# Kernel optimization log

Hardware: AMD Instinct MI355X
Metric: run time of the kernel (lower is better)

Reference implementation:

```python
import jax, jax.numpy as jnp
import numpy as np

BN_EPS = 1e-5
B, L, D = 16, 2048, 1024
OS = 64          # attnList[0]
NC = 256         # candidates per sample
CLASS_NUM = 8921
LAB = 1024


def setup_inputs() -> dict:
    key = jax.random.key(0)
    ks = jax.random.split(key, 8)
    scale_a = 1.0 / np.sqrt(D)
    return {
        "X": jax.random.normal(ks[0], (B, L, D), jnp.float32),
        "candidate": jax.random.randint(ks[1], (B, NC), 0, CLASS_NUM, jnp.int64),
        "a_w": jax.random.normal(ks[2], (D, OS), jnp.float32) * scale_a,
        "a_b": jnp.zeros((OS,), jnp.float32),
        "h_w": jax.random.normal(ks[3], (D, LAB), jnp.float32) * scale_a,
        "h_b": jnp.zeros((LAB,), jnp.float32),
        "bn_gamma": jax.random.uniform(ks[4], (LAB,), jnp.float32, 0.5, 1.5),
        "bn_beta": jax.random.normal(ks[5], (LAB,), jnp.float32) * 0.1,
        "bn_mean": jnp.zeros((LAB,), jnp.float32),
        "bn_var": jnp.ones((LAB,), jnp.float32),
        "labDescVec": jax.random.normal(ks[6], (CLASS_NUM, LAB), jnp.float32),
    }


def reference(X, candidate, a_w, a_b, h_w, h_b, bn_gamma, bn_beta, bn_mean, bn_var, labDescVec):
    # --- attention-pooling layer (attnList has one entry) ---
    # alpha: softmax over the sequence dim (dim=1 in torch)
    alpha = jax.nn.softmax(jnp.einsum('bld,do->blo', X, a_w) + a_b, axis=1)  # [B,L,OS]
    Xp = jnp.einsum('blo,bld->bod', alpha, X)                                # [B,OS,D]
    Xp = jnp.einsum('bod,dh->boh', Xp, h_w) + h_b                            # [B,OS,LAB]
    # BatchNorm1d over feature dim (eval mode: running stats)
    Xp = (Xp - bn_mean) * (bn_gamma / jnp.sqrt(bn_var + BN_EPS)) + bn_beta
    Xp = jax.nn.relu(Xp)  # dropout is identity at inference
    # --- candidate attention ---
    batchLabelVec = labDescVec[candidate]                                    # [B,NC,LAB]
    scores = jnp.einsum('boh,bch->boc', Xp, batchLabelVec)                   # [B,OS,NC]
    alpha2 = jax.nn.softmax(scores, axis=1)                                  # softmax over OS (dim=1)
    out = jnp.einsum('boc,boh->bch', alpha2, Xp)                             # [B,NC,LAB]
    return out
```

## Files before the change

kernel.cpp:

```cpp
#include <hip/hip_runtime.h>
#include <hip/hip_bf16.h>
#include <math.h>

#define Bb   16
#define Ll   2048
#define Dd   1024
#define OSo  64
#define NCc  256
#define LABh 1024
#define BN_EPS 1e-5f

typedef short s8v  __attribute__((ext_vector_type(8)));
typedef short s4v  __attribute__((ext_vector_type(4)));
typedef float f32x4 __attribute__((ext_vector_type(4)));

__device__ __forceinline__ short f2b(float f) {
    __hip_bfloat16 h = __float2bfloat16(f);
    short s;
    __builtin_memcpy(&s, &h, 2);
    return s;
}
__device__ __forceinline__ float b2f(short s) {
    union { unsigned u; float f; } v; v.u = ((unsigned)(unsigned short)s) << 16;
    return v.f;
}
__device__ __forceinline__ void fastbar() {
    asm volatile("s_waitcnt lgkmcnt(0)\n\ts_barrier" ::: "memory");
}
__device__ __forceinline__ int swi(int row, int kElem) {
    return (row * 128 + ((kElem * 2) ^ ((row & 7) << 4))) >> 1;
}
__device__ __forceinline__ f32x4 MF(s8v a, s8v b, f32x4 c) {
    return __builtin_amdgcn_mfma_f32_16x16x32_bf16(a, b, c, 0, 0, 0);
}

__global__ __launch_bounds__(256) void k0(const float* __restrict__ h_w,
                                          const float* __restrict__ a_w,
                                          short* __restrict__ h_wT,
                                          short* __restrict__ a_wT) {
    __shared__ float t[64][68];
    const int tid = threadIdx.x, id = blockIdx.x;
    const float* src; short* dst; int srw, d0, y0;
    if (id < 256) { src = h_w; dst = h_wT; srw = LABh; d0 = (id & 15) * 64; y0 = (id >> 4) * 64; }
    else          { src = a_w; dst = a_wT; srw = OSo;  d0 = (id - 256) * 64; y0 = 0; }
    const int r = tid >> 2, cofs = (tid & 3) * 16;
    #pragma unroll
    for (int w = 0; w < 4; ++w) {
        float4 v = *(const float4*)&src[(size_t)(d0 + r) * srw + y0 + cofs + w * 4];
        t[r][cofs + w * 4 + 0] = v.x;
        t[r][cofs + w * 4 + 1] = v.y;
        t[r][cofs + w * 4 + 2] = v.z;
        t[r][cofs + w * 4 + 3] = v.w;
    }
    __syncthreads();
    s8v o0, o1;
    #pragma unroll
    for (int e = 0; e < 8; ++e) { o0[e] = f2b(t[cofs + e][r]); o1[e] = f2b(t[cofs + 8 + e][r]); }
    *(s8v*)&dst[(size_t)(y0 + r) * Dd + d0 + cofs]     = o0;
    *(s8v*)&dst[(size_t)(y0 + r) * Dd + d0 + cofs + 8] = o1;
}

struct R1 { float4 x[4]; s8v w[2]; };

__global__ __launch_bounds__(256) void k1(const float* __restrict__ X,
                                          const short* __restrict__ a_wT,
                                          float* __restrict__ StP) {
    __shared__ __align__(16) char smem[32768];
    float (*ts)[65] = (float(*)[65])smem;
    const int tid = threadIdx.x;
    const int lane = tid & 63, wave = tid >> 6;
    const int wm = wave >> 1, wn = wave & 1;
    const int b = blockIdx.y, l0 = blockIdx.x * 64;
    const int z = blockIdx.z, kbase = z * 512;
    const float* Xb = X + ((size_t)b * Ll + l0) * Dd;
    const int r = tid >> 2, kofs = (tid & 3) * 16;
    f32x4 acc[2][2] = {};
    R1 cur, nxt;
    #pragma unroll
    for (int w = 0; w < 2; ++w) {
        cur.x[2*w]   = *(const float4*)&Xb[(size_t)r * Dd + kbase + kofs + w * 8];
        cur.x[2*w+1] = *(const float4*)&Xb[(size_t)r * Dd + kbase + kofs + w * 8 + 4];
        cur.w[w]     = *(const s8v*)&a_wT[(size_t)r * Dd + kbase + kofs + w * 8];
    }
    #pragma unroll
    for (int t = 0; t < 8; ++t) {
        short* As = (short*)(smem + (t & 1) * 8192);
        short* Bs = (short*)(smem + 16384 + (t & 1) * 8192);
        #pragma unroll
        for (int w = 0; w < 2; ++w) {
            const float* f0 = (const float*)&cur.x[2*w];
            s8v s;
            s[0]=f2b(f0[0]); s[1]=f2b(f0[1]); s[2]=f2b(f0[2]); s[3]=f2b(f0[3]);
            s[4]=f2b(f0[4]); s[5]=f2b(f0[5]); s[6]=f2b(f0[6]); s[7]=f2b(f0[7]);
            *(s8v*)&As[swi(r, kofs + w * 8)] = s;
            *(s8v*)&Bs[swi(r, kofs + w * 8)] = cur.w[w];
        }
        fastbar();
        if (t < 7) {
            const int k0 = kbase + (t + 1) * 64;
            #pragma unroll
            for (int w = 0; w < 2; ++w) {
                nxt.x[2*w]   = *(const float4*)&Xb[(size_t)r * Dd + k0 + kofs + w * 8];
                nxt.x[2*w+1] = *(const float4*)&Xb[(size_t)r * Dd + k0 + kofs + w * 8 + 4];
                nxt.w[w]     = *(const s8v*)&a_wT[(size_t)r * Dd + k0 + kofs + w * 8];
            }
        }
        #pragma unroll
        for (int kk = 0; kk < 2; ++kk) {
            const int kb = kk * 32 + (lane >> 4) * 8;
            s8v a[2], bb[2];
            #pragma unroll
            for (int i = 0; i < 2; ++i)
                a[i] = *(const s8v*)&As[swi(wm * 32 + i * 16 + (lane & 15), kb)];
            #pragma unroll
            for (int j = 0; j < 2; ++j)
                bb[j] = *(const s8v*)&Bs[swi(wn * 32 + j * 16 + (lane & 15), kb)];
            #pragma unroll
            for (int i = 0; i < 2; ++i)
                #pragma unroll
                for (int j = 0; j < 2; ++j)
                    acc[i][j] = MF(a[i], bb[j], acc[i][j]);
        }
        if (t < 7) cur = nxt;
    }
    __syncthreads();
    #pragma unroll
    for (int i = 0; i < 2; ++i)
        #pragma unroll
        for (int j = 0; j < 2; ++j)
            #pragma unroll
            for (int rr = 0; rr < 4; ++rr)
                ts[wm * 32 + i * 16 + (lane >> 4) * 4 + rr][wn * 32 + j * 16 + (lane & 15)] = acc[i][j][rr];
    __syncthreads();
    const int o = tid >> 2, lofs = (tid & 3) * 16;
    float* Sp = StP + (size_t)z * ((size_t)Bb * OSo * Ll)
                    + ((size_t)b * OSo + o) * Ll + l0 + lofs;
    #pragma unroll
    for (int w = 0; w < 4; ++w) {
        float4 v;
        v.x = ts[lofs + w * 4 + 0][o];
        v.y = ts[lofs + w * 4 + 1][o];
        v.z = ts[lofs + w * 4 + 2][o];
        v.w = ts[lofs + w * 4 + 3][o];
        *(float4*)&Sp[w * 4] = v;
    }
}

__global__ __launch_bounds__(256) void k2(const float* __restrict__ StP,
                                          const float* __restrict__ a_b,
                                          short* __restrict__ aBf) {
    __shared__ float row[Ll];
    __shared__ float red[8];
    const size_t ZS = (size_t)Bb * OSo * Ll;
    const float* p0 = StP + (size_t)blockIdx.x * Ll;
    const float* p1 = p0 + ZS;
    short* ab = aBf + (size_t)blockIdx.x * Ll;
    const int tid = threadIdx.x;
    const int wave = tid >> 6, lane = tid & 63;
    const float bias = a_b[blockIdx.x & (OSo - 1)];
    float m = -1e30f;
    for (int i = tid; i < Ll; i += 256) {
        float v = p0[i] + p1[i] + bias;
        row[i] = v; m = fmaxf(m, v);
    }
    #pragma unroll
    for (int off = 32; off; off >>= 1) m = fmaxf(m, __shfl_down(m, off));
    if (lane == 0) red[wave] = m;
    __syncthreads();
    if (tid == 0) red[4] = fmaxf(fmaxf(red[0], red[1]), fmaxf(red[2], red[3]));
    __syncthreads();
    const float M = red[4];
    float s = 0.f;
    for (int i = tid; i < Ll; i += 256) { float e = __expf(row[i] - M); row[i] = e; s += e; }
    __syncthreads();
    #pragma unroll
    for (int off = 32; off; off >>= 1) s += __shfl_down(s, off);
    if (lane == 0) red[wave] = s;
    __syncthreads();
    if (tid == 0) red[4] = 1.f / (red[0] + red[1] + red[2] + red[3]);
    __syncthreads();
    const float inv = red[4];
    for (int i = tid; i < Ll; i += 256) ab[i] = f2b(row[i] * inv);
}

struct R3 { s8v al[2]; float4 xv[4]; };

__global__ __launch_bounds__(256) void k3(const float* __restrict__ X,
                                          const short* __restrict__ aBf,
                                          float* __restrict__ XpP) {
    __shared__ __align__(16) char smem[32768];
    float (*ts)[68] = (float(*)[68])smem;
    const int tid = threadIdx.x;
    const int lane = tid & 63, wave = tid >> 6;
    const int wm = wave >> 1, wn = wave & 1;
    const int id = blockIdx.x;
    const int slot = id >> 3;
    const int b = (id & 7) * 2 + (slot >> 5);
    const int inner = slot & 31;
    const int dt = inner & 15, z = inner >> 4;
    const int d0 = dt * 64;
    const float* Xb = X + (size_t)b * Ll * Dd;
    const short* ab = aBf + (size_t)b * OSo * Ll;
    float* outP = XpP + (size_t)z * ((size_t)Bb * OSo * Dd);
    f32x4 acc[2][2] = {};
    const int arow = tid >> 2, akofs = (tid & 3) * 16;
    const int lq = tid & 15, dq = tid >> 4;
    const int lbase = z * 1024;
    R3 cur, nxt;
    #pragma unroll
    for (int w = 0; w < 2; ++w)
        cur.al[w] = *(const s8v*)&ab[(size_t)arow * Ll + lbase + akofs + w * 8];
    #pragma unroll
    for (int i = 0; i < 4; ++i)
        cur.xv[i] = *(const float4*)&Xb[(size_t)(lbase + lq * 4 + i) * Dd + d0 + dq * 4];
    #pragma unroll
    for (int t = 0; t < 16; ++t) {
        short* Aal = (short*)(smem + (t & 1) * 8192);
        short* Xs  = (short*)(smem + 16384 + (t & 1) * 8192);
        #pragma unroll
        for (int w = 0; w < 2; ++w)
            *(s8v*)&Aal[swi(arow, akofs + w * 8)] = cur.al[w];
        {
            const float* f = (const float*)cur.xv;
            #pragma unroll
            for (int j = 0; j < 4; ++j) {
                const int rowd = dq * 4 + j;
                s4v sj;
                sj[0] = f2b(f[0 * 4 + j]);
                sj[1] = f2b(f[1 * 4 + j]);
                sj[2] = f2b(f[2 * 4 + j]);
                sj[3] = f2b(f[3 * 4 + j]);
                *(s4v*)&Xs[swi(rowd, lq * 4)] = sj;
            }
        }
        fastbar();
        if (t < 15) {
            const int l0 = lbase + (t + 1) * 64;
            #pragma unroll
            for (int w = 0; w < 2; ++w)
                nxt.al[w] = *(const s8v*)&ab[(size_t)arow * Ll + l0 + akofs + w * 8];
            #pragma unroll
            for (int i = 0; i < 4; ++i)
                nxt.xv[i] = *(const float4*)&Xb[(size_t)(l0 + lq * 4 + i) * Dd + d0 + dq * 4];
        }
        #pragma unroll
        for (int kk = 0; kk < 2; ++kk) {
            const int kb = kk * 32 + (lane >> 4) * 8;
            s8v a[2], bb[2];
            #pragma unroll
            for (int i = 0; i < 2; ++i)
                a[i] = *(const s8v*)&Aal[swi(wm * 32 + i * 16 + (lane & 15), kb)];
            #pragma unroll
            for (int j = 0; j < 2; ++j)
                bb[j] = *(const s8v*)&Xs[swi(wn * 32 + j * 16 + (lane & 15), kb)];
            #pragma unroll
            for (int i = 0; i < 2; ++i)
                #pragma unroll
                for (int j = 0; j < 2; ++j)
                    acc[i][j] = MF(a[i], bb[j], acc[i][j]);
        }
        if (t < 15) cur = nxt;
    }
    __syncthreads();
    #pragma unroll
    for (int i = 0; i < 2; ++i)
        #pragma unroll
        for (int j = 0; j < 2; ++j)
            #pragma unroll
            for (int rr = 0; rr < 4; ++rr)
                ts[wm * 32 + i * 16 + (lane >> 4) * 4 + rr][wn * 32 + j * 16 + (lane & 15)] = acc[i][j][rr];
    __syncthreads();
    const int o = tid >> 2, dofs = (tid & 3) * 16;
    float* op = outP + ((size_t)b * OSo + o) * Dd + d0 + dofs;
    #pragma unroll
    for (int w = 0; w < 4; ++w)
        *(float4*)&op[w * 4] = *(float4*)&ts[o][dofs + w * 4];
}

struct R4 { float4 p[8]; s8v w[2]; };

__global__ __launch_bounds__(256) void k4(const float* __restrict__ XpP,
                                          const short* __restrict__ h_wT,
                                          const float* __restrict__ h_b,
                                          const float* __restrict__ gamma,
                                          const float* __restrict__ beta,
                                          const float* __restrict__ mean,
                                          const float* __restrict__ var,
                                          short* __restrict__ Xh) {
    __shared__ __align__(16) char smem[32768];
    short* tsb = (short*)smem;
    const int tid = threadIdx.x, lane = tid & 63, wave = tid >> 6;
    const int wm = wave >> 1, wn = wave & 1;
    const int h0 = blockIdx.x * 64, m0 = blockIdx.y * 64;
    const int r = tid >> 2, kofs = (tid & 3) * 16;
    const size_t ZS = (size_t)Bb * OSo * Dd;
    f32x4 acc[2][2] = {};
    R4 cur, nxt;
    #pragma unroll
    for (int w = 0; w < 2; ++w) {
        const float* p0 = XpP + (size_t)(m0 + r) * Dd + kofs + w * 8;
        cur.p[w*4+0] = *(const float4*)&p0[0];
        cur.p[w*4+1] = *(const float4*)&p0[4];
        cur.p[w*4+2] = *(const float4*)&p0[ZS];
        cur.p[w*4+3] = *(const float4*)&p0[ZS + 4];
        cur.w[w]     = *(const s8v*)&h_wT[(size_t)(h0 + r) * Dd + kofs + w * 8];
    }
    #pragma unroll
    for (int t = 0; t < 16; ++t) {
        short* As = (short*)(smem + (t & 1) * 8192);
        short* Bs = (short*)(smem + 16384 + (t & 1) * 8192);
        #pragma unroll
        for (int w = 0; w < 2; ++w) {
            const float* f0 = (const float*)&cur.p[w*4];
            const float* f1 = (const float*)&cur.p[w*4+2];
            s8v s;
            #pragma unroll
            for (int e = 0; e < 8; ++e) s[e] = f2b(f0[e] + f1[e]);
            *(s8v*)&As[swi(r, kofs + w * 8)] = s;
            *(s8v*)&Bs[swi(r, kofs + w * 8)] = cur.w[w];
        }
        fastbar();
        if (t < 15) {
            const int k0 = (t + 1) * 64;
            #pragma unroll
            for (int w = 0; w < 2; ++w) {
                const float* p0 = XpP + (size_t)(m0 + r) * Dd + k0 + kofs + w * 8;
                nxt.p[w*4+0] = *(const float4*)&p0[0];
                nxt.p[w*4+1] = *(const float4*)&p0[4];
                nxt.p[w*4+2] = *(const float4*)&p0[ZS];
                nxt.p[w*4+3] = *(const float4*)&p0[ZS + 4];
                nxt.w[w]     = *(const s8v*)&h_wT[(size_t)(h0 + r) * Dd + k0 + kofs + w * 8];
            }
        }
        #pragma unroll
        for (int kk = 0; kk < 2; ++kk) {
            const int kb = kk * 32 + (lane >> 4) * 8;
            s8v a[2], bb[2];
            #pragma unroll
            for (int i = 0; i < 2; ++i)
                a[i] = *(const s8v*)&As[swi(wm * 32 + i * 16 + (lane & 15), kb)];
            #pragma unroll
            for (int j = 0; j < 2; ++j)
                bb[j] = *(const s8v*)&Bs[swi(wn * 32 + j * 16 + (lane & 15), kb)];
            #pragma unroll
            for (int i = 0; i < 2; ++i)
                #pragma unroll
                for (int j = 0; j < 2; ++j)
                    acc[i][j] = MF(a[i], bb[j], acc[i][j]);
        }
        if (t < 15) cur = nxt;
    }
    __syncthreads();
    #pragma unroll
    for (int j = 0; j < 2; ++j) {
        const int h = h0 + wn * 32 + j * 16 + (lane & 15);
        const float sc = gamma[h] * rsqrtf(var[h] + BN_EPS);
        const float of = (h_b[h] - mean[h]) * sc + beta[h];
        #pragma unroll
        for (int i = 0; i < 2; ++i)
            #pragma unroll
            for (int rr = 0; rr < 4; ++rr) {
                const int ml = wm * 32 + i * 16 + (lane >> 4) * 4 + rr;
                tsb[ml * 64 + wn * 32 + j * 16 + (lane & 15)] = f2b(fmaxf(0.f, acc[i][j][rr] * sc + of));
            }
    }
    __syncthreads();
    #pragma unroll
    for (int w = 0; w < 2; ++w)
        *(s8v*)&Xh[(size_t)(m0 + r) * LABh + h0 + kofs + w * 8] = *(const s8v*)&tsb[r * 64 + kofs + w * 8];
}

struct R5 { float4 ld[4]; s8v xh[2]; };

__global__ __launch_bounds__(256) void k5(const int* __restrict__ cand,
                                          const float* __restrict__ labD,
                                          const short* __restrict__ Xh,
                                          float* __restrict__ scP) {
    __shared__ __align__(16) char smem[33024];
    float (*ts)[68] = (float(*)[68])smem;
    int* cidx = (int*)(smem + 32768);
    const int tid = threadIdx.x, lane = tid & 63, wave = tid >> 6;
    const int wm = wave >> 1, wn = wave & 1;
    const int b = blockIdx.y;
    const int ct = blockIdx.x & 3, z = blockIdx.x >> 2;
    const int c0 = ct * 64;
    const int kbase = z * 256;
    if (tid < 64) cidx[tid] = cand[b * NCc + c0 + tid];
    __syncthreads();
    const int r = tid >> 2, kofs = (tid & 3) * 16;
    const int ci = cidx[r];
    const float* lrow = labD + (size_t)ci * LABh + kbase;
    const short* xrow = Xh + (size_t)(b * OSo + r) * LABh + kbase;
    f32x4 acc[2][2] = {};
    R5 cur, nxt;
    #pragma unroll
    for (int w = 0; w < 2; ++w) {
        cur.ld[2*w]   = *(const float4*)&lrow[kofs + w * 8];
        cur.ld[2*w+1] = *(const float4*)&lrow[kofs + w * 8 + 4];
        cur.xh[w]     = *(const s8v*)&xrow[kofs + w * 8];
    }
    #pragma unroll
    for (int t = 0; t < 4; ++t) {
        short* As = (short*)(smem + (t & 1) * 8192);
        short* Bs = (short*)(smem + 16384 + (t & 1) * 8192);
        #pragma unroll
        for (int w = 0; w < 2; ++w) {
            const float* f0 = (const float*)&cur.ld[2*w];
            s8v s;
            #pragma unroll
            for (int e = 0; e < 8; ++e) s[e] = f2b(f0[e]);
            *(s8v*)&As[swi(r, kofs + w * 8)] = s;
            *(s8v*)&Bs[swi(r, kofs + w * 8)] = cur.xh[w];
        }
        fastbar();
        if (t < 3) {
            const int k0 = (t + 1) * 64;
            #pragma unroll
            for (int w = 0; w < 2; ++w) {
                nxt.ld[2*w]   = *(const float4*)&lrow[k0 + kofs + w * 8];
                nxt.ld[2*w+1] = *(const float4*)&lrow[k0 + kofs + w * 8 + 4];
                nxt.xh[w]     = *(const s8v*)&xrow[k0 + kofs + w * 8];
            }
        }
        #pragma unroll
        for (int kk = 0; kk < 2; ++kk) {
            const int kb = kk * 32 + (lane >> 4) * 8;
            s8v a[2], bb[2];
            #pragma unroll
            for (int i = 0; i < 2; ++i)
                a[i] = *(const s8v*)&As[swi(wm * 32 + i * 16 + (lane & 15), kb)];
            #pragma unroll
            for (int j = 0; j < 2; ++j)
                bb[j] = *(const s8v*)&Bs[swi(wn * 32 + j * 16 + (lane & 15), kb)];
            #pragma unroll
            for (int i = 0; i < 2; ++i)
                #pragma unroll
                for (int j = 0; j < 2; ++j)
                    acc[i][j] = MF(a[i], bb[j], acc[i][j]);
        }
        if (t < 3) cur = nxt;
    }
    __syncthreads();
    #pragma unroll
    for (int i = 0; i < 2; ++i)
        #pragma unroll
        for (int j = 0; j < 2; ++j)
            #pragma unroll
            for (int rr = 0; rr < 4; ++rr)
                ts[wm * 32 + i * 16 + (lane >> 4) * 4 + rr][wn * 32 + j * 16 + (lane & 15)] = acc[i][j][rr];
    __syncthreads();
    const int oofs = (tid & 3) * 16;
    float* sp = scP + (size_t)z * ((size_t)Bb * NCc * OSo)
                    + ((size_t)b * NCc + c0 + r) * OSo + oofs;
    #pragma unroll
    for (int w = 0; w < 4; ++w)
        *(float4*)&sp[w * 4] = *(float4*)&ts[r][oofs + w * 4];
}

__global__ __launch_bounds__(256) void k6(const float* __restrict__ scP,
                                          const short* __restrict__ Xh,
                                          float* __restrict__ out) {
    __shared__ float al[8][64];
    const int tid = threadIdx.x;
    const int id = blockIdx.x;
    const int slot = id >> 3;
    const int b = (id & 7) * 2 + (slot >> 5);
    const int c0 = (slot & 31) * 8;
    const size_t ZS = (size_t)Bb * NCc * OSo;
    {
        const int cl = tid >> 5, t32 = tid & 31;
        const float* srow = scP + ((size_t)b * NCc + c0 + cl) * OSo;
        float v[2];
        float m = -1e30f;
        #pragma unroll
        for (int j = 0; j < 2; ++j) {
            const int o = t32 + j * 32;
            v[j] = srow[o] + srow[ZS + o] + srow[2 * ZS + o] + srow[3 * ZS + o];
            m = fmaxf(m, v[j]);
        }
        #pragma unroll
        for (int off = 16; off; off >>= 1) m = fmaxf(m, __shfl_xor(m, off, 32));
        float s = 0.f;
        #pragma unroll
        for (int j = 0; j < 2; ++j) { v[j] = __expf(v[j] - m); s += v[j]; }
        #pragma unroll
        for (int off = 16; off; off >>= 1) s += __shfl_xor(s, off, 32);
        float inv = 1.f / s;
        #pragma unroll
        for (int j = 0; j < 2; ++j) al[cl][t32 + j * 32] = v[j] * inv;
    }
    __syncthreads();
    const short* xb = Xh + (size_t)b * OSo * LABh;
    float acc[8][4] = {};
    for (int o = 0; o < OSo; ++o) {
        s4v xv = *(const s4v*)&xb[(size_t)o * LABh + tid * 4];
        const float x0 = b2f(xv[0]), x1 = b2f(xv[1]), x2 = b2f(xv[2]), x3 = b2f(xv[3]);
        #pragma unroll
        for (int c = 0; c < 8; ++c) {
            const float w = al[c][o];
            acc[c][0] += w * x0; acc[c][1] += w * x1; acc[c][2] += w * x2; acc[c][3] += w * x3;
        }
    }
    #pragma unroll
    for (int c = 0; c < 8; ++c) {
        float4 v; v.x = acc[c][0]; v.y = acc[c][1]; v.z = acc[c][2]; v.w = acc[c][3];
        *(float4*)&out[((size_t)b * NCc + c0 + c) * LABh + tid * 4] = v;
    }
}

extern "C" void kernel_launch(void* const* d_in, const int* in_sizes, int n_in,
                              void* d_out, int out_size, void* d_ws, size_t ws_size,
                              hipStream_t stream) {
    (void)in_sizes; (void)n_in; (void)out_size; (void)ws_size;
    const float* X      = (const float*)d_in[0];
    const int*   cand   = (const int*)  d_in[1];
    const float* a_w    = (const float*)d_in[2];
    const float* a_b    = (const float*)d_in[3];
    const float* h_w    = (const float*)d_in[4];
    const float* h_b    = (const float*)d_in[5];
    const float* gamma  = (const float*)d_in[6];
    const float* beta   = (const float*)d_in[7];
    const float* mean   = (const float*)d_in[8];
    const float* var    = (const float*)d_in[9];
    const float* labDesc= (const float*)d_in[10];
    float* outp = (float*)d_out;

    char* ws = (char*)d_ws;
    float* StP  = (float*)ws;
    float* XpP  = (float*)ws;
    short* aBf  = (short*)(ws + ((size_t)16 << 20));
    short* Xh   = (short*)(ws + ((size_t)20 << 20));
    float* scP  = (float*)(ws + ((size_t)22 << 20));
    short* a_wT = (short*)(ws + ((size_t)26 << 20));
    short* h_wT = (short*)(ws + ((size_t)27 << 20));

    k0 <<<272,              256, 0, stream>>>(h_w, a_w, h_wT, a_wT);
    k1 <<<dim3(32, 16, 2),  256, 0, stream>>>(X, a_wT, StP);
    k2 <<<Bb * OSo,         256, 0, stream>>>(StP, a_b, aBf);
    k3 <<<512,              256, 0, stream>>>(X, aBf, XpP);
    k4 <<<dim3(16, 16),     256, 0, stream>>>(XpP, h_wT, h_b, gamma, beta, mean, var, Xh);
    k5 <<<dim3(16, 16),     256, 0, stream>>>(cand, labDesc, Xh, scP);
    k6 <<<512,              256, 0, stream>>>(scP, Xh, outp);
}
```

Baseline: 110.5 us.

## Fuse candidate score GEMM with softmax and weighted sum; vectorize alpha softmax

Merges the candidate-score kernel (k5) and the softmax/weighted-sum kernel (k6) into one kernel, k56. Each block computes scores for 16 candidates over the full LAB dimension, applies softmax over OS in shared memory, and then accumulates the output. This removes the split-K partial score buffer, its global round trip and one launch, at the cost of a small-tile GEMM with only one MFMA per wave per k-step and 256 blocks. The sequence softmax kernel k2 also switches to float4 loads and stores.

Result: faster. 106.2 us (-3.9%).

```diff
diff --git a/kernel.cpp b/kernel.cpp
--- a/kernel.cpp
+++ b/kernel.cpp
@@ -158,10 +158,17 @@
     const int tid = threadIdx.x;
     const int wave = tid >> 6, lane = tid & 63;
     const float bias = a_b[blockIdx.x & (OSo - 1)];
+    const int base = tid * 4;
     float m = -1e30f;
-    for (int i = tid; i < Ll; i += 256) {
-        float v = p0[i] + p1[i] + bias;
-        row[i] = v; m = fmaxf(m, v);
+    #pragma unroll
+    for (int i = base; i < Ll; i += 1024) {
+        float4 a = *(const float4*)&p0[i];
+        float4 c = *(const float4*)&p1[i];
+        float4 v;
+        v.x = a.x + c.x + bias; v.y = a.y + c.y + bias;
+        v.z = a.z + c.z + bias; v.w = a.w + c.w + bias;
+        *(float4*)&row[i] = v;
+        m = fmaxf(m, fmaxf(fmaxf(v.x, v.y), fmaxf(v.z, v.w)));
     }
     #pragma unroll
     for (int off = 32; off; off >>= 1) m = fmaxf(m, __shfl_down(m, off));
@@ -171,7 +178,14 @@
     __syncthreads();
     const float M = red[4];
     float s = 0.f;
-    for (int i = tid; i < Ll; i += 256) { float e = __expf(row[i] - M); row[i] = e; s += e; }
+    #pragma unroll
+    for (int i = base; i < Ll; i += 1024) {
+        float4 v = *(const float4*)&row[i];
+        v.x = __expf(v.x - M); v.y = __expf(v.y - M);
+        v.z = __expf(v.z - M); v.w = __expf(v.w - M);
+        *(float4*)&row[i] = v;
+        s += (v.x + v.y) + (v.z + v.w);
+    }
     __syncthreads();
     #pragma unroll
     for (int off = 32; off; off >>= 1) s += __shfl_down(s, off);
@@ -180,7 +194,14 @@
     if (tid == 0) red[4] = 1.f / (red[0] + red[1] + red[2] + red[3]);
     __syncthreads();
     const float inv = red[4];
-    for (int i = tid; i < Ll; i += 256) ab[i] = f2b(row[i] * inv);
+    #pragma unroll
+    for (int i = base; i < Ll; i += 1024) {
+        float4 v = *(const float4*)&row[i];
+        s4v o;
+        o[0] = f2b(v.x * inv); o[1] = f2b(v.y * inv);
+        o[2] = f2b(v.z * inv); o[3] = f2b(v.w * inv);
+        *(s4v*)&ab[i] = o;
+    }
 }
 
 struct R3 { s8v al[2]; float4 xv[4]; };
@@ -370,141 +391,99 @@
         *(s8v*)&Xh[(size_t)(m0 + r) * LABh + h0 + kofs + w * 8] = *(const s8v*)&tsb[r * 64 + kofs + w * 8];
 }
 
-struct R5 { float4 ld[4]; s8v xh[2]; };
-
-__global__ __launch_bounds__(256) void k5(const int* __restrict__ cand,
-                                          const float* __restrict__ labD,
-                                          const short* __restrict__ Xh,
-                                          float* __restrict__ scP) {
-    __shared__ __align__(16) char smem[33024];
+struct R56 { float4 ld; s8v xh[2]; };
+
+__global__ __launch_bounds__(256) void k56(const int* __restrict__ cand,
+                                           const float* __restrict__ labD,
+                                           const short* __restrict__ Xh,
+                                           float* __restrict__ out) {
+    __shared__ __align__(16) char smem[20608];
     float (*ts)[68] = (float(*)[68])smem;
-    int* cidx = (int*)(smem + 32768);
+    float (*al)[64] = (float(*)[64])(smem + 4608);
+    int* cidx = (int*)(smem + 20480);
     const int tid = threadIdx.x, lane = tid & 63, wave = tid >> 6;
-    const int wm = wave >> 1, wn = wave & 1;
-    const int b = blockIdx.y;
-    const int ct = blockIdx.x & 3, z = blockIdx.x >> 2;
-    const int c0 = ct * 64;
-    const int kbase = z * 256;
-    if (tid < 64) cidx[tid] = cand[b * NCc + c0 + tid];
-    __syncthreads();
-    const int r = tid >> 2, kofs = (tid & 3) * 16;
-    const int ci = cidx[r];
-    const float* lrow = labD + (size_t)ci * LABh + kbase;
-    const short* xrow = Xh + (size_t)(b * OSo + r) * LABh + kbase;
-    f32x4 acc[2][2] = {};
-    R5 cur, nxt;
-    #pragma unroll
-    for (int w = 0; w < 2; ++w) {
-        cur.ld[2*w]   = *(const float4*)&lrow[kofs + w * 8];
-        cur.ld[2*w+1] = *(const float4*)&lrow[kofs + w * 8 + 4];
-        cur.xh[w]     = *(const s8v*)&xrow[kofs + w * 8];
-    }
-    #pragma unroll
-    for (int t = 0; t < 4; ++t) {
-        short* As = (short*)(smem + (t & 1) * 8192);
-        short* Bs = (short*)(smem + 16384 + (t & 1) * 8192);
-        #pragma unroll
-        for (int w = 0; w < 2; ++w) {
-            const float* f0 = (const float*)&cur.ld[2*w];
-            s8v s;
-            #pragma unroll
-            for (int e = 0; e < 8; ++e) s[e] = f2b(f0[e]);
-            *(s8v*)&As[swi(r, kofs + w * 8)] = s;
-            *(s8v*)&Bs[swi(r, kofs + w * 8)] = cur.xh[w];
+    const int id = blockIdx.x;
+    const int slot = id >> 3;
+    const int b = (id & 7) * 2 + (slot >> 4);
+    const int c0 = (slot & 15) * 16;
+    if (tid < 16) cidx[tid] = cand[b * NCc + c0 + tid];
+    __syncthreads();
+    const int ar = tid >> 4, ak = (tid & 15) * 4;
+    const int br = tid >> 2, bk = (tid & 3) * 16;
+    const float* lrow = labD + (size_t)cidx[ar] * LABh;
+    const short* xb = Xh + (size_t)b * OSo * LABh;
+    f32x4 acc = {};
+    R56 cur, nxt;
+    cur.ld    = *(const float4*)&lrow[ak];
+    cur.xh[0] = *(const s8v*)&xb[(size_t)br * LABh + bk];
+    cur.xh[1] = *(const s8v*)&xb[(size_t)br * LABh + bk + 8];
+    #pragma unroll
+    for (int t = 0; t < 16; ++t) {
+        short* As = (short*)(smem + (t & 1) * 10240);
+        short* Bs = As + 1024;
+        {
+            s4v sa;
+            sa[0] = f2b(cur.ld.x); sa[1] = f2b(cur.ld.y);
+            sa[2] = f2b(cur.ld.z); sa[3] = f2b(cur.ld.w);
+            *(s4v*)&As[swi(ar, ak)] = sa;
+            *(s8v*)&Bs[swi(br, bk)]     = cur.xh[0];
+            *(s8v*)&Bs[swi(br, bk + 8)] = cur.xh[1];
         }
         fastbar();
-        if (t < 3) {
+        if (t < 15) {
             const int k0 = (t + 1) * 64;
-            #pragma unroll
-            for (int w = 0; w < 2; ++w) {
-                nxt.ld[2*w]   = *(const float4*)&lrow[k0 + kofs + w * 8];
-                nxt.ld[2*w+1] = *(const float4*)&lrow[k0 + kofs + w * 8 + 4];
-                nxt.xh[w]     = *(const s8v*)&xrow[k0 + kofs + w * 8];
-            }
+            nxt.ld    = *(const float4*)&lrow[k0 + ak];
+            nxt.xh[0] = *(const s8v*)&xb[(size_t)br * LABh + k0 + bk];
+            nxt.xh[1] = *(const s8v*)&xb[(size_t)br * LABh + k0 + bk + 8];
         }
         #pragma unroll
         for (int kk = 0; kk < 2; ++kk) {
             const int kb = kk * 32 + (lane >> 4) * 8;
-            s8v a[2], bb[2];
-            #pragma unroll
-            for (int i = 0; i < 2; ++i)
-                a[i] = *(const s8v*)&As[swi(wm * 32 + i * 16 + (lane & 15), kb)];
-            #pragma unroll
-            for (int j = 0; j < 2; ++j)
-                bb[j] = *(const s8v*)&Bs[swi(wn * 32 + j * 16 + (lane & 15), kb)];
-            #pragma unroll
-            for (int i = 0; i < 2; ++i)
-                #pragma unroll
-                for (int j = 0; j < 2; ++j)
-                    acc[i][j] = MF(a[i], bb[j], acc[i][j]);
-        }
-        if (t < 3) cur = nxt;
-    }
-    __syncthreads();
-    #pragma unroll
-    for (int i = 0; i < 2; ++i)
-        #pragma unroll
-        for (int j = 0; j < 2; ++j)
-            #pragma unroll
-            for (int rr = 0; rr < 4; ++rr)
-                ts[wm * 32 + i * 16 + (lane >> 4) * 4 + rr][wn * 32 + j * 16 + (lane & 15)] = acc[i][j][rr];
-    __syncthreads();
-    const int oofs = (tid & 3) * 16;
-    float* sp = scP + (size_t)z * ((size_t)Bb * NCc * OSo)
-                    + ((size_t)b * NCc + c0 + r) * OSo + oofs;
-    #pragma unroll
-    for (int w = 0; w < 4; ++w)
-        *(float4*)&sp[w * 4] = *(float4*)&ts[r][oofs + w * 4];
-}
-
-__global__ __launch_bounds__(256) void k6(const float* __restrict__ scP,
-                                          const short* __restrict__ Xh,
-                                          float* __restrict__ out) {
-    __shared__ float al[8][64];
-    const int tid = threadIdx.x;
-    const int id = blockIdx.x;
-    const int slot = id >> 3;
-    const int b = (id & 7) * 2 + (slot >> 5);
-    const int c0 = (slot & 31) * 8;
-    const size_t ZS = (size_t)Bb * NCc * OSo;
+            s8v a  = *(const s8v*)&As[swi(lane & 15, kb)];
+            s8v bv = *(const s8v*)&Bs[swi(wave * 16 + (lane & 15), kb)];
+            acc = MF(a, bv, acc);
+        }
+        if (t < 15) cur = nxt;
+    }
+    __syncthreads();
+    #pragma unroll
+    for (int rr = 0; rr < 4; ++rr)
+        ts[(lane >> 4) * 4 + rr][wave * 16 + (lane & 15)] = acc[rr];
+    __syncthreads();
     {
-        const int cl = tid >> 5, t32 = tid & 31;
-        const float* srow = scP + ((size_t)b * NCc + c0 + cl) * OSo;
-        float v[2];
+        const int cl = tid >> 4, t16 = tid & 15;
+        float v[4];
         float m = -1e30f;
         #pragma unroll
-        for (int j = 0; j < 2; ++j) {
-            const int o = t32 + j * 32;
-            v[j] = srow[o] + srow[ZS + o] + srow[2 * ZS + o] + srow[3 * ZS + o];
-            m = fmaxf(m, v[j]);
-        }
-        #pragma unroll
-        for (int off = 16; off; off >>= 1) m = fmaxf(m, __shfl_xor(m, off, 32));
+        for (int j = 0; j < 4; ++j) { v[j] = ts[cl][t16 + j * 16]; m = fmaxf(m, v[j]); }
+        #pragma unroll
+        for (int off = 8; off; off >>= 1) m = fmaxf(m, __shfl_xor(m, off, 16));
         float s = 0.f;
         #pragma unroll
-        for (int j = 0; j < 2; ++j) { v[j] = __expf(v[j] - m); s += v[j]; }
-        #pragma unroll
-        for (int off = 16; off; off >>= 1) s += __shfl_xor(s, off, 32);
-        float inv = 1.f / s;
-        #pragma unroll
-        for (int j = 0; j < 2; ++j) al[cl][t32 + j * 32] = v[j] * inv;
-    }
-    __syncthreads();
-    const short* xb = Xh + (size_t)b * OSo * LABh;
-    float acc[8][4] = {};
+        for (int j = 0; j < 4; ++j) { v[j] = __expf(v[j] - m); s += v[j]; }
+        #pragma unroll
+        for (int off = 8; off; off >>= 1) s += __shfl_xor(s, off, 16);
+        const float inv = 1.f / s;
+        #pragma unroll
+        for (int j = 0; j < 4; ++j) al[cl][t16 + j * 16] = v[j] * inv;
+    }
+    __syncthreads();
+    const int h0 = tid * 4;
+    float acc2[16][4] = {};
     for (int o = 0; o < OSo; ++o) {
-        s4v xv = *(const s4v*)&xb[(size_t)o * LABh + tid * 4];
+        s4v xv = *(const s4v*)&xb[(size_t)o * LABh + h0];
         const float x0 = b2f(xv[0]), x1 = b2f(xv[1]), x2 = b2f(xv[2]), x3 = b2f(xv[3]);
         #pragma unroll
-        for (int c = 0; c < 8; ++c) {
+        for (int c = 0; c < 16; ++c) {
             const float w = al[c][o];
-            acc[c][0] += w * x0; acc[c][1] += w * x1; acc[c][2] += w * x2; acc[c][3] += w * x3;
-        }
-    }
-    #pragma unroll
-    for (int c = 0; c < 8; ++c) {
-        float4 v; v.x = acc[c][0]; v.y = acc[c][1]; v.z = acc[c][2]; v.w = acc[c][3];
-        *(float4*)&out[((size_t)b * NCc + c0 + c) * LABh + tid * 4] = v;
+            acc2[c][0] += w * x0; acc2[c][1] += w * x1;
+            acc2[c][2] += w * x2; acc2[c][3] += w * x3;
+        }
+    }
+    #pragma unroll
+    for (int c = 0; c < 16; ++c) {
+        float4 v; v.x = acc2[c][0]; v.y = acc2[c][1]; v.z = acc2[c][2]; v.w = acc2[c][3];
+        *(float4*)&out[((size_t)b * NCc + c0 + c) * LABh + h0] = v;
     }
 }
 
@@ -530,7 +509,6 @@
     float* XpP  = (float*)ws;
     short* aBf  = (short*)(ws + ((size_t)16 << 20));
     short* Xh   = (short*)(ws + ((size_t)20 << 20));
-    float* scP  = (float*)(ws + ((size_t)22 << 20));
     short* a_wT = (short*)(ws + ((size_t)26 << 20));
     short* h_wT = (short*)(ws + ((size_t)27 << 20));
 
@@ -539,6 +517,5 @@
     k2 <<<Bb * OSo,         256, 0, stream>>>(StP, a_b, aBf);
     k3 <<<512,              256, 0, stream>>>(X, aBf, XpP);
     k4 <<<dim3(16, 16),     256, 0, stream>>>(XpP, h_wT, h_b, gamma, beta, mean, var, Xh);
-    k5 <<<dim3(16, 16),     256, 0, stream>>>(cand, labDesc, Xh, scP);
-    k6 <<<512,              256, 0, stream>>>(scP, Xh, outp);
-}
+    k56<<<256,              256, 0, stream>>>(cand, labDesc, Xh, outp);
+}
```
